# Kernel optimization log

Hardware: AMD Instinct MI355X
Metric: run time of the kernel (lower is better)

## Reference

```python
import jax, jax.numpy as jnp
import numpy as np

B, S, E = 8, 2048, 1024
EPS = 1e-5

def _layernorm(x, w, b):
    mu = jnp.mean(x, axis=-1, keepdims=True)
    var = jnp.mean(jnp.square(x - mu), axis=-1, keepdims=True)
    return (x - mu) * jax.lax.rsqrt(var + EPS) * w + b

def setup_inputs() -> dict:
    key = jax.random.key(0)
    ks = jax.random.split(key, 12)
    x = jax.random.normal(ks[0], (B, S, E), dtype=jnp.float32)
    pad_mask = jax.random.randint(ks[1], (B, 1, S), 0, 2).astype(bool)
    pad_mask = pad_mask.at[:, :, 0].set(False)  # ensure no fully-masked row
    s = 1.0 / np.sqrt(E)
    Wq = jax.random.normal(ks[2], (E, E), jnp.float32) * s
    Wk = jax.random.normal(ks[3], (E, E), jnp.float32) * s
    Wv = jax.random.normal(ks[4], (E, E), jnp.float32) * s
    bq = jnp.zeros((E,), jnp.float32)
    bk = jnp.zeros((E,), jnp.float32)
    bv = jnp.zeros((E,), jnp.float32)
    W1 = jax.random.normal(ks[5], (2 * E, E), jnp.float32) * s
    b1 = jnp.zeros((2 * E,), jnp.float32)
    W2 = jax.random.normal(ks[6], (E, 2 * E), jnp.float32) * (1.0 / np.sqrt(2 * E))
    b2 = jnp.zeros((E,), jnp.float32)
    ln1_w = jnp.ones((E,), jnp.float32); ln1_b = jnp.zeros((E,), jnp.float32)
    ln2_w = jnp.ones((E,), jnp.float32); ln2_b = jnp.zeros((E,), jnp.float32)
    return {"x": x, "pad_mask": pad_mask, "ln1_w": ln1_w, "ln1_b": ln1_b,
            "ln2_w": ln2_w, "ln2_b": ln2_b, "Wq": Wq, "bq": bq, "Wk": Wk,
            "bk": bk, "Wv": Wv, "bv": bv, "W1": W1, "b1": b1, "W2": W2, "b2": b2}

def reference(x, pad_mask, ln1_w, ln1_b, ln2_w, ln2_b, Wq, bq, Wk, bk, Wv, bv, W1, b1, W2, b2):
    scale = jnp.sqrt(jnp.float32(x.shape[-1]))
    normed = _layernorm(x, ln1_w, ln1_b)
    Q = jnp.einsum('bse,de->bsd', normed, Wq) + bq
    K = jnp.einsum('bse,de->bsd', normed, Wk) + bk
    V = jnp.einsum('bse,de->bsd', normed, Wv) + bv
    scores = jnp.einsum('bqd,bkd->bqk', Q, K) / scale  # [B,S,S]
    scores = jnp.where(pad_mask, -jnp.inf, scores)
    attn = jax.nn.softmax(scores, axis=2)  # dropout is identity at inference
    x = x + jnp.einsum('bqk,bkd->bqd', attn, V)
    h = _layernorm(x, ln2_w, ln2_b)
    h = jax.nn.relu(jnp.einsum('bse,fe->bsf', h, W1) + b1)
    x = x + jnp.einsum('bsf,ef->bse', h, W2) + b2
    return x
```

## Files before the change

### kernel.cpp

```cpp
#include <hip/hip_runtime.h>
#include <hip/hip_bf16.h>
#include <cstdint>

#define B_ 8
#define S_ 2048
#define E_ 1024

using u16 = unsigned short;

typedef __bf16 bf16x8 __attribute__((ext_vector_type(8)));
typedef float f32x4 __attribute__((ext_vector_type(4)));

__device__ inline u16 f2bf(float f) {
  uint32_t u = __float_as_uint(f);
  uint32_t r = (u + 0x7fffu + ((u >> 16) & 1u)) >> 16;
  return (u16)r;
}

template<bool HAS_BIAS, bool RELU, bool HAS_RES, bool OUT_BF16, bool SCORES,
         bool GATHER_A, bool RUNTK>
__global__ __launch_bounds__(512, 2) void gemm_nt(
    const u16* __restrict__ A, const u16* __restrict__ B, void* __restrict__ C,
    const float* __restrict__ bias, const float* __restrict__ res,
    int lda, int ldb, int ldc, int K,
    long long strideA, long long strideB, long long strideC,
    const int* __restrict__ cidx, const int* __restrict__ cnt)
{
  __shared__ __attribute__((aligned(16))) u16 lA[2][2][128 * 64];
  __shared__ __attribute__((aligned(16))) u16 lB[2][2][128 * 64];

  const int tid  = threadIdx.x;
  const int lane = tid & 63;
  const int wave = tid >> 6;

  const int GM = 8, GN = 4;
  const int nbn = gridDim.x, nbm = gridDim.y, nz = gridDim.z;
  int bm, bn, bz;
  {
    const int total = nbn * nbm * nz;
    const long long lin = blockIdx.x +
        (long long)nbn * (blockIdx.y + (long long)nbm * blockIdx.z);
    if ((nbm % GM) == 0 && (nbn % GN) == 0 && (total % (8 * GM * GN)) == 0) {
      const int xcd = (int)(lin & 7);
      const int loc = (int)(lin >> 3);
      const int sper = GM * GN;
      const int super = (loc / sper) * 8 + xcd;
      const int ins   = loc % sper;
      const int spz = (nbm / GM) * (nbn / GN);
      bz = super / spz;
      const int s2 = super % spz;
      const int sm = s2 % (nbm / GM);
      const int sn = s2 / (nbm / GM);
      bm = sm * GM + (ins % GM);
      bn = sn * GN + (ins / GM);
    } else { bm = blockIdx.y; bn = blockIdx.x; bz = blockIdx.z; }
  }

  int count = 0, cpad = 0;
  if (SCORES || GATHER_A || RUNTK) {
    count = cnt[bz * 2];
    cpad  = cnt[bz * 2 + 1];
    if (GATHER_A && bm * 256 >= cpad) return;
    if (SCORES   && bn * 256 >= cpad) return;
  }
  const int Keff = RUNTK ? cpad : K;
  const int nk = Keff >> 6;

  const u16* Ab = A + (long long)bz * strideA;
  const u16* Bb = B + (long long)bz * strideB;

  const int srow = tid >> 3;
  const int scol = ((tid & 7) ^ (srow & 7)) * 8;
  long long rowA[2][2], rowB[2][2];
#pragma unroll
  for (int h = 0; h < 2; ++h)
#pragma unroll
    for (int l = 0; l < 2; ++l) {
      int ra = bm * 256 + h * 128 + srow + l * 64;
      if (GATHER_A) ra = cidx[(long long)bz * S_ + ra];
      rowA[h][l] = (long long)ra * lda + scol;
      rowB[h][l] = (long long)(bn * 256 + h * 128 + srow + l * 64) * ldb + scol;
    }
  const int ldsoff0 = tid * 8;
  const int ldsoff1 = (tid + 512) * 8;

  const int wr = wave >> 2, wc = wave & 3;
  const int rA = wr * 64 + (lane & 15);
  const int rB = wc * 32 + (lane & 15);
#define LDSP3(P) ((uint32_t)(uintptr_t)(__attribute__((address_space(3))) const void*)(P))
  uint32_t aA0 = LDSP3(&lA[0][0][0]) +
      2u * (uint32_t)(rA * 64 + (((0 * 4 + (lane >> 4)) ^ (rA & 7)) * 8));
  uint32_t aA1 = LDSP3(&lA[0][0][0]) +
      2u * (uint32_t)(rA * 64 + (((1 * 4 + (lane >> 4)) ^ (rA & 7)) * 8));
  uint32_t bB0 = LDSP3(&lB[0][0][0]) +
      2u * (uint32_t)(rB * 64 + (((0 * 4 + (lane >> 4)) ^ (rB & 7)) * 8));
  uint32_t bB1 = LDSP3(&lB[0][0][0]) +
      2u * (uint32_t)(rB * 64 + (((1 * 4 + (lane >> 4)) ^ (rB & 7)) * 8));
#undef LDSP3

  f32x4 acc[2][2][4][2];
#pragma unroll
  for (int a = 0; a < 2; ++a)
#pragma unroll
    for (int b = 0; b < 2; ++b)
#pragma unroll
      for (int mi = 0; mi < 4; ++mi)
#pragma unroll
        for (int ni = 0; ni < 2; ++ni)
          acc[a][b][mi][ni] = (f32x4){0.f, 0.f, 0.f, 0.f};

#define STAGE_A(H, T) {                                                        \
    const int tt_ = ((T) < nk) ? (T) : (nk - 1);                               \
    __builtin_amdgcn_global_load_lds(                                          \
        (const __attribute__((address_space(1))) void*)                        \
            (Ab + rowA[H][0] + (long long)tt_ * 64),                           \
        (__attribute__((address_space(3))) void*)(&lA[(T) & 1][H][ldsoff0]),   \
        16, 0, 0);                                                             \
    __builtin_amdgcn_global_load_lds(                                          \
        (const __attribute__((address_space(1))) void*)                        \
            (Ab + rowA[H][1] + (long long)tt_ * 64),                           \
        (__attribute__((address_space(3))) void*)(&lA[(T) & 1][H][ldsoff1]),   \
        16, 0, 0); }

#define STAGE_B(H, T) {                                                        \
    const int tt_ = ((T) < nk) ? (T) : (nk - 1);                               \
    __builtin_amdgcn_global_load_lds(                                          \
        (const __attribute__((address_space(1))) void*)                        \
            (Bb + rowB[H][0] + (long long)tt_ * 64),                           \
        (__attribute__((address_space(3))) void*)(&lB[(T) & 1][H][ldsoff0]),   \
        16, 0, 0);                                                             \
    __builtin_amdgcn_global_load_lds(                                          \
        (const __attribute__((address_space(1))) void*)                        \
            (Bb + rowB[H][1] + (long long)tt_ * 64),                           \
        (__attribute__((address_space(3))) void*)(&lB[(T) & 1][H][ldsoff1]),   \
        16, 0, 0); }

#define DSR(D, ADDR, OFF) \
    asm volatile("ds_read_b128 %0, %1 offset:" OFF : "=v"(D) : "v"(ADDR))

#define LOADA0() { \
    DSR(af[0][0], aA0, "0");     DSR(af[0][1], aA1, "0");                      \
    DSR(af[1][0], aA0, "2048");  DSR(af[1][1], aA1, "2048");                   \
    DSR(af[2][0], aA0, "4096");  DSR(af[2][1], aA1, "4096");                   \
    DSR(af[3][0], aA0, "6144");  DSR(af[3][1], aA1, "6144"); }

#define LOADA1() { \
    DSR(af[0][0], aA0, "16384"); DSR(af[0][1], aA1, "16384");                  \
    DSR(af[1][0], aA0, "18432"); DSR(af[1][1], aA1, "18432");                  \
    DSR(af[2][0], aA0, "20480"); DSR(af[2][1], aA1, "20480");                  \
    DSR(af[3][0], aA0, "22528"); DSR(af[3][1], aA1, "22528"); }

#define LOADB0() { \
    DSR(bfv[0][0], bB0, "0");     DSR(bfv[0][1], bB1, "0");                    \
    DSR(bfv[1][0], bB0, "2048");  DSR(bfv[1][1], bB1, "2048"); }

#define LOADB1() { \
    DSR(bfv[0][0], bB0, "16384"); DSR(bfv[0][1], bB1, "16384");                \
    DSR(bfv[1][0], bB0, "18432"); DSR(bfv[1][1], bB1, "18432"); }

#define MFMAQ(MH, NH) {                                                        \
    __builtin_amdgcn_s_setprio(1);                                             \
    _Pragma("unroll") for (int mi = 0; mi < 4; ++mi)                           \
      _Pragma("unroll") for (int ni = 0; ni < 2; ++ni)                         \
        _Pragma("unroll") for (int k2 = 0; k2 < 2; ++k2)                       \
          acc[MH][NH][mi][ni] = __builtin_amdgcn_mfma_f32_16x16x32_bf16(       \
              af[mi][k2], bfv[ni][k2], acc[MH][NH][mi][ni], 0, 0, 0);          \
    __builtin_amdgcn_s_setprio(0); }

#define BAR()    __builtin_amdgcn_s_barrier()
#define LGKM0()  asm volatile("s_waitcnt lgkmcnt(0)" ::: "memory")
#define SCHED0() __builtin_amdgcn_sched_barrier(0)

  STAGE_A(0, 0); STAGE_B(0, 0); STAGE_A(1, 0); STAGE_B(1, 0);
  STAGE_A(0, 1); STAGE_B(1, 1);
  asm volatile("s_waitcnt vmcnt(4)" ::: "memory");
  BAR();

  bf16x8 af[4][2], bfv[2][2];
  for (int t = 0; t < nk; ++t) {
    STAGE_A(1, t + 1);
    LOADA0(); LOADB0();
    BAR(); LGKM0(); SCHED0();
    MFMAQ(0, 0);
    BAR();
    STAGE_B(0, t + 1);
    LOADB1();
    BAR(); LGKM0(); SCHED0();
    MFMAQ(0, 1);
    BAR();
    STAGE_A(0, t + 2);
    LOADA1();
    BAR(); LGKM0(); SCHED0();
    MFMAQ(1, 1);
    BAR();
    STAGE_B(1, t + 2);
    LOADB0();
    BAR(); LGKM0(); SCHED0();
    MFMAQ(1, 0);
    asm volatile("s_waitcnt vmcnt(4)" ::: "memory");
    BAR();
    const uint32_t d = (t & 1) ? (uint32_t)-32768 : 32768u;
    aA0 += d; aA1 += d; bB0 += d; bB1 += d;
  }
  asm volatile("s_waitcnt vmcnt(0)" ::: "memory");

#undef MFMAQ
#undef LOADA0
#undef LOADA1
#undef LOADB0
#undef LOADB1
#undef DSR
#undef STAGE_A
#undef STAGE_B
#undef BAR
#undef LGKM0
#undef SCHED0

  const float* resb = (const float*)C;
  if (HAS_RES) resb = res + (long long)bz * strideC;
  u16*   cb16 = (u16*)C   + (long long)bz * strideC;
  float* cf32 = (float*)C + (long long)bz * strideC;

#pragma unroll
  for (int mh = 0; mh < 2; ++mh)
#pragma unroll
  for (int nh = 0; nh < 2; ++nh)
#pragma unroll
  for (int ni = 0; ni < 2; ++ni) {
    const int gn = bn * 256 + nh * 128 + wc * 32 + ni * 16 + (lane & 15);
    const float bvv = HAS_BIAS ? bias[gn] : 0.f;
    const bool cmask = SCORES && (gn >= count);
#pragma unroll
    for (int mi = 0; mi < 4; ++mi) {
#pragma unroll
      for (int r = 0; r < 4; ++r) {
        const int gm = bm * 256 + mh * 128 + wr * 64 + mi * 16 + (lane >> 4) * 4 + r;
        const long long idx = (long long)gm * ldc + gn;
        float v = acc[mh][nh][mi][ni][r] + bvv;
        if (SCORES) { v *= 0.03125f; if (cmask) v = -3.0e38f; }
        if (RELU) v = fmaxf(v, 0.f);
        if (HAS_RES) v += resb[idx];
        if (OUT_BF16) cb16[idx] = f2bf(v);
        else          cf32[idx] = v;
      }
    }
  }
}

__global__ __launch_bounds__(256) void layernorm_kernel(
    const float* __restrict__ x, const float* __restrict__ w,
    const float* __restrict__ b, u16* __restrict__ out)
{
  const int row = blockIdx.x;
  const int tid = threadIdx.x;
  const float4 v = ((const float4*)(x + (long long)row * E_))[tid];
  float s  = v.x + v.y + v.z + v.w;
  float s2 = v.x * v.x + v.y * v.y + v.z * v.z + v.w * v.w;
#pragma unroll
  for (int o = 32; o >= 1; o >>= 1) { s += __shfl_xor(s, o); s2 += __shfl_xor(s2, o); }
  __shared__ float rs[4], rs2[4];
  const int wave = tid >> 6, lane = tid & 63;
  if (lane == 0) { rs[wave] = s; rs2[wave] = s2; }
  __syncthreads();
  s  = rs[0] + rs[1] + rs[2] + rs[3];
  s2 = rs2[0] + rs2[1] + rs2[2] + rs2[3];
  const float mu   = s * (1.f / E_);
  const float var  = s2 * (1.f / E_) - mu * mu;
  const float rstd = rsqrtf(var + 1e-5f);
  const float4 wv = ((const float4*)w)[tid];
  const float4 bv = ((const float4*)b)[tid];
  ushort4 o;
  o.x = f2bf((v.x - mu) * rstd * wv.x + bv.x);
  o.y = f2bf((v.y - mu) * rstd * wv.y + bv.y);
  o.z = f2bf((v.z - mu) * rstd * wv.z + bv.z);
  o.w = f2bf((v.w - mu) * rstd * wv.w + bv.w);
  ((ushort4*)(out + (long long)row * E_))[tid] = o;
}

__global__ __launch_bounds__(256) void softmax_bf16_kernel(
    u16* __restrict__ sp, const int* __restrict__ cnt)
{
  const int row = blockIdx.x;
  const int bz  = row >> 11;
  const int tid = threadIdx.x;
  const int cpad = cnt[bz * 2 + 1];
  const bool act = (tid * 8) < cpad;
  u16* pr = sp + (long long)row * S_;

  float v[8];
  if (act) {
    const uint4 raw = ((const uint4*)pr)[tid];
    const uint32_t w[4] = {raw.x, raw.y, raw.z, raw.w};
#pragma unroll
    for (int c = 0; c < 4; ++c) {
      v[2 * c]     = __uint_as_float(w[c] << 16);
      v[2 * c + 1] = __uint_as_float(w[c] & 0xffff0000u);
    }
  } else {
#pragma unroll
    for (int i = 0; i < 8; ++i) v[i] = -3.38e38f;
  }
  float mx = -3.38e38f;
#pragma unroll
  for (int i = 0; i < 8; ++i) mx = fmaxf(mx, v[i]);
#pragma unroll
  for (int o = 32; o >= 1; o >>= 1) mx = fmaxf(mx, __shfl_xor(mx, o));
  __shared__ float red[4];
  const int wave = tid >> 6, lane = tid & 63;
  if (lane == 0) red[wave] = mx;
  __syncthreads();
  mx = fmaxf(fmaxf(red[0], red[1]), fmaxf(red[2], red[3]));

  float s = 0.f;
#pragma unroll
  for (int i = 0; i < 8; ++i) { v[i] = __expf(v[i] - mx); s += v[i]; }
#pragma unroll
  for (int o = 32; o >= 1; o >>= 1) s += __shfl_xor(s, o);
  __syncthreads();
  if (lane == 0) red[wave] = s;
  __syncthreads();
  s = red[0] + red[1] + red[2] + red[3];
  const float inv = 1.f / s;

  if (act) {
    uint4 o4;
    uint32_t* ow = (uint32_t*)&o4;
#pragma unroll
    for (int c = 0; c < 4; ++c) {
      const uint32_t lo = f2bf(v[2 * c] * inv);
      const uint32_t hi = f2bf(v[2 * c + 1] * inv);
      ow[c] = lo | (hi << 16);
    }
    ((uint4*)pr)[tid] = o4;
  }
}

__global__ __launch_bounds__(256) void transpose_kernel(
    const u16* __restrict__ KVc, u16* __restrict__ Vt, const int* __restrict__ cnt)
{
  const int bl = blockIdx.z;
  const int s0 = blockIdx.y * 32;
  if (s0 >= cnt[bl * 2 + 1]) return;
  __shared__ u16 tile[32][33];
  const int e0 = blockIdx.x * 32;
  const int tx = threadIdx.x & 31, ty = threadIdx.x >> 5;
  const u16* src = KVc + ((long long)bl * S_ + s0) * (2 * E_) + E_ + e0;
#pragma unroll
  for (int r = 0; r < 32; r += 8)
    tile[ty + r][tx] = src[(long long)(ty + r) * (2 * E_) + tx];
  __syncthreads();
  u16* dst = Vt + ((long long)bl * E_ + e0) * S_ + s0;
#pragma unroll
  for (int r = 0; r < 32; r += 8)
    dst[(long long)(ty + r) * S_ + tx] = tile[tx][ty + r];
}

__global__ __launch_bounds__(256) void prep_kernel(
    const float* __restrict__ Wq, const float* __restrict__ Wk,
    const float* __restrict__ Wv, const float* __restrict__ W1,
    const float* __restrict__ W2, const float* __restrict__ bk,
    const float* __restrict__ bv,
    u16* __restrict__ Wqb, u16* __restrict__ Wkvb,
    u16* __restrict__ W1b, u16* __restrict__ W2b, float* __restrict__ bkv)
{
  const int N1 = E_ * E_;
  const long long i = (long long)blockIdx.x * 256 + threadIdx.x;
  if (i < N1)               Wqb[i] = f2bf(Wq[i]);
  else if (i < 2LL * N1)    Wkvb[i - N1] = f2bf(Wk[i - N1]);
  else if (i < 3LL * N1)    Wkvb[N1 + (i - 2LL * N1)] = f2bf(Wv[i - 2LL * N1]);
  else if (i < 5LL * N1)    W1b[i - 3LL * N1] = f2bf(W1[i - 3LL * N1]);
  else if (i < 7LL * N1)    W2b[i - 5LL * N1] = f2bf(W2[i - 5LL * N1]);
  else if (i < 7LL * N1 + 2 * E_) {
    const int j = (int)(i - 7LL * N1);
    bkv[j] = (j < E_) ? bk[j] : bv[j - E_];
  }
}

__global__ void detect_kernel(const unsigned char* __restrict__ m, int* __restrict__ flag)
{
  __shared__ int any;
  if (threadIdx.x == 0) any = 0;
  __syncthreads();
  int loc = 0;
  for (int i = threadIdx.x; i < B_ * S_; i += 256)
    if ((i & 3) && m[i]) loc = 1;
  if (loc) atomicOr(&any, 1);
  __syncthreads();
  if (threadIdx.x == 0) *flag = any;
}

__global__ __launch_bounds__(256) void compact_kernel(
    const void* __restrict__ mask, const int* __restrict__ flag,
    int* __restrict__ cidx, int* __restrict__ cnt)
{
  const int b = blockIdx.x;
  const int tid = threadIdx.x, lane = tid & 63, wave = tid >> 6;
  const bool u8m = (*flag != 0);
  const unsigned char* m8 = (const unsigned char*)mask + (long long)b * S_;
  const int* m32 = (const int*)mask + (long long)b * S_;

  int keep[8]; int my = 0;
#pragma unroll
  for (int j = 0; j < 8; ++j) {
    const int s = tid * 8 + j;
    const bool k = u8m ? (m8[s] == 0) : (m32[s] == 0);
    keep[j] = k ? 1 : 0; my += keep[j];
  }
  int pre = my;
#pragma unroll
  for (int o = 1; o < 64; o <<= 1) {
    const int n = __shfl_up(pre, o);
    if (lane >= o) pre += n;
  }
  __shared__ int wsum[4];
  if (lane == 63) wsum[wave] = pre;
  __syncthreads();
  int wbase = 0;
#pragma unroll
  for (int w = 0; w < 4; ++w) if (w < wave) wbase += wsum[w];
  int pos = wbase + pre - my;
  int* cx = cidx + (long long)b * S_;
#pragma unroll
  for (int j = 0; j < 8; ++j)
    if (keep[j]) cx[pos++] = tid * 8 + j;
  const int total = wsum[0] + wsum[1] + wsum[2] + wsum[3];
  const int cpad = (total + 255) & ~255;
  for (int i = total + tid; i < cpad; i += 256) cx[i] = 0;
  if (tid == 0) { cnt[b * 2] = total; cnt[b * 2 + 1] = cpad; }
}

extern "C" void kernel_launch(void* const* d_in, const int* in_sizes, int n_in,
                              void* d_out, int out_size, void* d_ws, size_t ws_size,
                              hipStream_t stream)
{
  const float* x    = (const float*)d_in[0];
  const void*  mask = d_in[1];
  const float* ln1w = (const float*)d_in[2];
  const float* ln1b = (const float*)d_in[3];
  const float* ln2w = (const float*)d_in[4];
  const float* ln2b = (const float*)d_in[5];
  const float* Wq   = (const float*)d_in[6];
  const float* bq   = (const float*)d_in[7];
  const float* Wk   = (const float*)d_in[8];
  const float* bk   = (const float*)d_in[9];
  const float* Wv   = (const float*)d_in[10];
  const float* bv   = (const float*)d_in[11];
  const float* W1   = (const float*)d_in[12];
  const float* b1   = (const float*)d_in[13];
  const float* W2   = (const float*)d_in[14];
  const float* b2   = (const float*)d_in[15];

  const size_t MB = 1024ull * 1024ull;
  char* p = (char*)d_ws;
  int* flag    = (int*)p;   p += 256;
  int* cnt     = (int*)p;   p += 256;
  int* cidx    = (int*)p;   p += (size_t)B_ * S_ * 4;
  u16* Wqb     = (u16*)p;   p += (size_t)E_ * E_ * 2;
  u16* Wkvb    = (u16*)p;   p += (size_t)2 * E_ * E_ * 2;
  u16* W1b     = (u16*)p;   p += (size_t)2 * E_ * E_ * 2;
  u16* W2b     = (u16*)p;   p += (size_t)2 * E_ * E_ * 2;
  float* bkv   = (float*)p; p += 2 * E_ * 4;
  u16* normedb = (u16*)p;   p += (size_t)B_ * S_ * E_ * 2;
  char* chunk  = p;
  const size_t used  = (size_t)(p - (char*)d_ws);
  const size_t avail = (ws_size > used) ? (ws_size - used) : 0;

  int bc = 1;
  for (int c = 8; c >= 1; c >>= 1)
    if (avail >= 24 * MB * (size_t)c) { bc = c; break; }

  float* out = (float*)d_out;
  dim3 blk(256);
  dim3 blkg(512);

  detect_kernel<<<1, 256, 0, stream>>>((const unsigned char*)mask, flag);
  compact_kernel<<<B_, blk, 0, stream>>>(mask, flag, cidx, cnt);
  {
    const long long tot = 7LL * E_ * E_ + 2 * E_;
    prep_kernel<<<(int)((tot + 255) / 256), blk, 0, stream>>>(
        Wq, Wk, Wv, W1, W2, bk, bv, Wqb, Wkvb, W1b, W2b, bkv);
  }

  layernorm_kernel<<<B_ * S_, blk, 0, stream>>>(x, ln1w, ln1b, normedb);

  for (int b0 = 0; b0 < B_; b0 += bc) {
    u16* Qc  = (u16*)chunk;
    u16* KVc = Qc + (size_t)bc * S_ * E_;
    u16* Vt  = KVc + (size_t)bc * S_ * 2 * E_;
    u16* Pc  = Vt + (size_t)bc * E_ * S_;
    const int* cntb  = cnt + b0 * 2;
    const int* cidxb = cidx + (size_t)b0 * S_;

    gemm_nt<true, false, false, true, false, false, false>
        <<<dim3(E_ / 256, bc * S_ / 256, 1), blkg, 0, stream>>>(
        normedb + (size_t)b0 * S_ * E_, Wqb, Qc, bq, nullptr,
        E_, E_, E_, E_, 0, 0, 0, nullptr, nullptr);

    gemm_nt<true, false, false, true, false, true, false>
        <<<dim3(2 * E_ / 256, S_ / 256, bc), blkg, 0, stream>>>(
        normedb + (size_t)b0 * S_ * E_, Wkvb, KVc, bkv, nullptr,
        E_, E_, 2 * E_, E_,
        (long long)S_ * E_, 0, (long long)S_ * 2 * E_, cidxb, cntb);

    transpose_kernel<<<dim3(E_ / 32, S_ / 32, bc), blk, 0, stream>>>(KVc, Vt, cntb);

    gemm_nt<false, false, false, true, true, false, false>
        <<<dim3(S_ / 256, S_ / 256, bc), blkg, 0, stream>>>(
        Qc, KVc, Pc, nullptr, nullptr,
        E_, 2 * E_, S_, E_,
        (long long)S_ * E_, (long long)S_ * 2 * E_, (long long)S_ * S_,
        nullptr, cntb);

    softmax_bf16_kernel<<<bc * S_, blk, 0, stream>>>(Pc, cntb);

    gemm_nt<false, false, true, false, false, false, true>
        <<<dim3(E_ / 256, S_ / 256, bc), blkg, 0, stream>>>(
        Pc, Vt, out + (size_t)b0 * S_ * E_, nullptr,
        x + (size_t)b0 * S_ * E_, S_, S_, E_, S_,
        (long long)S_ * S_, (long long)E_ * S_, (long long)S_ * E_,
        nullptr, cntb);
  }

  layernorm_kernel<<<B_ * S_, blk, 0, stream>>>(out, ln2w, ln2b, normedb);

  size_t mr_sz = avail / ((size_t)2 * E_ * 2);
  int mr = (int)((mr_sz > 16384) ? 16384 : mr_sz);
  mr &= ~255;
  if (mr < 256) mr = 256;
  u16* hb = (u16*)chunk;
  for (int m0 = 0; m0 < B_ * S_; m0 += mr) {
    const int mm = (B_ * S_ - m0 < mr) ? (B_ * S_ - m0) : mr;
    gemm_nt<true, true, false, true, false, false, false>
        <<<dim3((2 * E_) / 256, mm / 256, 1), blkg, 0, stream>>>(
        normedb + (size_t)m0 * E_, W1b, hb, b1, nullptr,
        E_, E_, 2 * E_, E_, 0, 0, 0, nullptr, nullptr);
    gemm_nt<true, false, true, false, false, false, false>
        <<<dim3(E_ / 256, mm / 256, 1), blkg, 0, stream>>>(
        hb, W2b, out + (size_t)m0 * E_, b2, out + (size_t)m0 * E_,
        2 * E_, 2 * E_, E_, 2 * E_, 0, 0, 0, nullptr, nullptr);
  }
}
```

Baseline: 639.3 us.

## Interleave LDS fragment reads with MFMAs using partial lgkmcnt waits

```diff
diff --git a/kernel.cpp b/kernel.cpp
--- a/kernel.cpp
+++ b/kernel.cpp
@@ -138,65 +138,67 @@
 #define DSR(D, ADDR, OFF) \
     asm volatile("ds_read_b128 %0, %1 offset:" OFF : "=v"(D) : "v"(ADDR))
 
-#define LOADA0() { \
-    DSR(af[0][0], aA0, "0");     DSR(af[0][1], aA1, "0");                      \
-    DSR(af[1][0], aA0, "2048");  DSR(af[1][1], aA1, "2048");                   \
-    DSR(af[2][0], aA0, "4096");  DSR(af[2][1], aA1, "4096");                   \
-    DSR(af[3][0], aA0, "6144");  DSR(af[3][1], aA1, "6144"); }
-
-#define LOADA1() { \
-    DSR(af[0][0], aA0, "16384"); DSR(af[0][1], aA1, "16384");                  \
-    DSR(af[1][0], aA0, "18432"); DSR(af[1][1], aA1, "18432");                  \
-    DSR(af[2][0], aA0, "20480"); DSR(af[2][1], aA1, "20480");                  \
-    DSR(af[3][0], aA0, "22528"); DSR(af[3][1], aA1, "22528"); }
-
-#define LOADB0() { \
-    DSR(bfv[0][0], bB0, "0");     DSR(bfv[0][1], bB1, "0");                    \
-    DSR(bfv[1][0], bB0, "2048");  DSR(bfv[1][1], bB1, "2048"); }
-
-#define LOADB1() { \
-    DSR(bfv[0][0], bB0, "16384"); DSR(bfv[0][1], bB1, "16384");                \
-    DSR(bfv[1][0], bB0, "18432"); DSR(bfv[1][1], bB1, "18432"); }
-
-#define MFMAQ(MH, NH) {                                                        \
-    __builtin_amdgcn_s_setprio(1);                                             \
-    _Pragma("unroll") for (int mi = 0; mi < 4; ++mi)                           \
-      _Pragma("unroll") for (int ni = 0; ni < 2; ++ni)                         \
-        _Pragma("unroll") for (int k2 = 0; k2 < 2; ++k2)                       \
-          acc[MH][NH][mi][ni] = __builtin_amdgcn_mfma_f32_16x16x32_bf16(       \
-              af[mi][k2], bfv[ni][k2], acc[MH][NH][mi][ni], 0, 0, 0);          \
-    __builtin_amdgcn_s_setprio(0); }
-
-#define BAR()    __builtin_amdgcn_s_barrier()
-#define LGKM0()  asm volatile("s_waitcnt lgkmcnt(0)" ::: "memory")
-#define SCHED0() __builtin_amdgcn_sched_barrier(0)
+#define LGKM(NSTR) asm volatile("s_waitcnt lgkmcnt(" NSTR ")" ::: "memory")
+#define SCHED0()   __builtin_amdgcn_sched_barrier(0)
+#define BAR()      __builtin_amdgcn_s_barrier()
+
+#define MFMA_MI(MH, NH, MI, BF) {                                              \
+    _Pragma("unroll") for (int ni = 0; ni < 2; ++ni)                           \
+      _Pragma("unroll") for (int k2 = 0; k2 < 2; ++k2)                         \
+        acc[MH][NH][MI][ni] = __builtin_amdgcn_mfma_f32_16x16x32_bf16(         \
+            af[MI][k2], BF[ni][k2], acc[MH][NH][MI][ni], 0, 0, 0); }
 
   STAGE_A(0, 0); STAGE_B(0, 0); STAGE_A(1, 0); STAGE_B(1, 0);
   STAGE_A(0, 1); STAGE_B(1, 1);
   asm volatile("s_waitcnt vmcnt(4)" ::: "memory");
   BAR();
 
-  bf16x8 af[4][2], bfv[2][2];
+  bf16x8 af[4][2], bfv[2][2], bfv2[2][2];
   for (int t = 0; t < nk; ++t) {
+    DSR(af[0][0], aA0, "0");      DSR(af[0][1], aA1, "0");
+    DSR(bfv[0][0], bB0, "0");     DSR(bfv[0][1], bB1, "0");
+    DSR(bfv[1][0], bB0, "2048");  DSR(bfv[1][1], bB1, "2048");
+    DSR(af[1][0], aA0, "2048");   DSR(af[1][1], aA1, "2048");
+    DSR(af[2][0], aA0, "4096");   DSR(af[2][1], aA1, "4096");
+    DSR(af[3][0], aA0, "6144");   DSR(af[3][1], aA1, "6144");
+    DSR(bfv2[0][0], bB0, "16384"); DSR(bfv2[0][1], bB1, "16384");
+    DSR(bfv2[1][0], bB0, "18432"); DSR(bfv2[1][1], bB1, "18432");
     STAGE_A(1, t + 1);
-    LOADA0(); LOADB0();
-    BAR(); LGKM0(); SCHED0();
-    MFMAQ(0, 0);
+    BAR();
+    __builtin_amdgcn_s_setprio(1);
+    LGKM("10"); SCHED0(); MFMA_MI(0, 0, 0, bfv);
+    LGKM("8");  SCHED0(); MFMA_MI(0, 0, 1, bfv);
+    LGKM("6");  SCHED0(); MFMA_MI(0, 0, 2, bfv);
+    LGKM("4");  SCHED0(); MFMA_MI(0, 0, 3, bfv);
+    __builtin_amdgcn_s_setprio(0);
     BAR();
     STAGE_B(0, t + 1);
-    LOADB1();
-    BAR(); LGKM0(); SCHED0();
-    MFMAQ(0, 1);
-    BAR();
+    BAR();
+    LGKM("0"); SCHED0();
+    __builtin_amdgcn_s_setprio(1);
+    MFMA_MI(0, 1, 0, bfv2); MFMA_MI(0, 1, 1, bfv2);
+    MFMA_MI(0, 1, 2, bfv2); MFMA_MI(0, 1, 3, bfv2);
+    __builtin_amdgcn_s_setprio(0);
+    BAR();
+    DSR(af[0][0], aA0, "16384"); DSR(af[0][1], aA1, "16384");
+    DSR(af[1][0], aA0, "18432"); DSR(af[1][1], aA1, "18432");
+    DSR(af[2][0], aA0, "20480"); DSR(af[2][1], aA1, "20480");
+    DSR(af[3][0], aA0, "22528"); DSR(af[3][1], aA1, "22528");
     STAGE_A(0, t + 2);
-    LOADA1();
-    BAR(); LGKM0(); SCHED0();
-    MFMAQ(1, 1);
+    BAR();
+    __builtin_amdgcn_s_setprio(1);
+    LGKM("6"); SCHED0(); MFMA_MI(1, 1, 0, bfv2);
+    LGKM("4"); SCHED0(); MFMA_MI(1, 1, 1, bfv2);
+    LGKM("2"); SCHED0(); MFMA_MI(1, 1, 2, bfv2);
+    LGKM("0"); SCHED0(); MFMA_MI(1, 1, 3, bfv2);
+    __builtin_amdgcn_s_setprio(0);
     BAR();
     STAGE_B(1, t + 2);
-    LOADB0();
-    BAR(); LGKM0(); SCHED0();
-    MFMAQ(1, 0);
+    BAR();
+    __builtin_amdgcn_s_setprio(1);
+    MFMA_MI(1, 0, 0, bfv); MFMA_MI(1, 0, 1, bfv);
+    MFMA_MI(1, 0, 2, bfv); MFMA_MI(1, 0, 3, bfv);
+    __builtin_amdgcn_s_setprio(0);
     asm volatile("s_waitcnt vmcnt(4)" ::: "memory");
     BAR();
     const uint32_t d = (t & 1) ? (uint32_t)-32768 : 32768u;
@@ -204,16 +206,12 @@
   }
   asm volatile("s_waitcnt vmcnt(0)" ::: "memory");
 
-#undef MFMAQ
-#undef LOADA0
-#undef LOADA1
-#undef LOADB0
-#undef LOADB1
+#undef MFMA_MI
 #undef DSR
 #undef STAGE_A
 #undef STAGE_B
 #undef BAR
-#undef LGKM0
+#undef LGKM
 #undef SCHED0
 
   const float* resb = (const float*)C;
```

Result: faster. 625.7 us (-2.1%).
